# Performance work log

Measured on AMD Instinct MI355X. Metric: run time of the kernel, lower is better.

## Reference

```python
import jax, jax.numpy as jnp
import numpy as np

N_NODES = 100000
DEG = 16
N_FEAT = 128
HID = 128
N_CLASSES = 16
BATCH = 10000


def setup_inputs() -> dict:
    key = jax.random.key(0)
    k1, k2, k3, k4, k5 = jax.random.split(key, 5)
    nodes = jax.random.randint(k1, (BATCH,), 0, N_NODES, dtype=jnp.int32)
    neigh_idx = jax.random.randint(k2, (N_NODES, DEG), 0, N_NODES, dtype=jnp.int32)
    features = jax.random.normal(k3, (N_NODES, N_FEAT), dtype=jnp.float32)
    W1 = jax.random.normal(k4, (HID, 2 * N_FEAT), dtype=jnp.float32) * 0.05
    W2 = jax.random.normal(k5, (N_CLASSES, 2 * HID), dtype=jnp.float32) * 0.05
    return {"nodes": nodes, "neigh_idx": neigh_idx, "features": features,
            "W1": W1, "W2": W2}


def reference(nodes, neigh_idx, features, W1, W2):
    # --- layer 1 (full graph): mean-aggregate neighbors, concat self, linear, relu
    neigh1 = jnp.take(features, neigh_idx, axis=0).mean(axis=1)      # [N, F]
    comb1 = jnp.concatenate([features, neigh1], axis=1)              # [N, 2F]
    h1 = jax.nn.relu(comb1 @ W1.T)                                   # [N, HID]
    # --- layer 2 (batch nodes only)
    batch_nbrs = jnp.take(neigh_idx, nodes, axis=0)                  # [B, deg]
    neigh2 = jnp.take(h1, batch_nbrs, axis=0).mean(axis=1)           # [B, HID]
    self2 = jnp.take(h1, nodes, axis=0)                              # [B, HID]
    comb2 = jnp.concatenate([self2, neigh2], axis=1)                 # [B, 2*HID]
    return comb2 @ W2.T                                              # [B, C]
```

## Files before the change

### kernel.cpp

```cpp
#include <hip/hip_runtime.h>
#include <hip/hip_bf16.h>

#define NN 100000
#define DEG 16
#define NF 128
#define HID 128
#define NC 16
#define NB 10000

#define AS1 __attribute__((address_space(1)))
#define AS3 __attribute__((address_space(3)))

typedef float f32x16 __attribute__((ext_vector_type(16)));
typedef short s16x8 __attribute__((ext_vector_type(8)));

__device__ __forceinline__ ushort f2bf(float f) {
    unsigned u = __builtin_bit_cast(unsigned, f);
    return (ushort)((u + 0x7FFFu + ((u >> 16) & 1u)) >> 16);
}
__device__ __forceinline__ float bf2f(ushort h) {
    return __builtin_bit_cast(float, (unsigned)h << 16);
}
__device__ __forceinline__ uint cvtpk(float a, float b) {
    uint r;
    asm("v_cvt_pk_bf16_f32 %0, %1, %2" : "=v"(r) : "v"(a), "v"(b));
    return r;
}
__device__ __forceinline__ s16x8 pack8(float4 a, float4 b) {
    uint4 u;
    u.x = cvtpk(a.x, a.y);
    u.y = cvtpk(a.z, a.w);
    u.z = cvtpk(b.x, b.y);
    u.w = cvtpk(b.z, b.w);
    return __builtin_bit_cast(s16x8, u);
}
__device__ __forceinline__ int swz16(int row, int bo) {
    return row * 256 + (bo ^ ((row & 15) << 4));
}
__device__ __forceinline__ uint swzA(uint row, uint bo) {
    return bo ^ ((row & 31u) << 4);
}
__device__ __forceinline__ int pi_feat(int p) {
    const int n = p >> 5, h = (p >> 4) & 1, g = p & 15;
    return 32 * n + 4 * h + (g & 3) + 8 * (g >> 2);
}

__global__ __launch_bounds__(256)
void wf_prep(const float* __restrict__ W1, const float* __restrict__ W2,
             ushort* __restrict__ WFh, ushort* __restrict__ WF2) {
    const int t = blockIdx.x * 256 + threadIdx.x;
    if (t >= 72 * 64) return;
    const int frag = t >> 6;
    const int lane = t & 63;
    const int k0 = (frag & 7) * 16 + (lane >> 5) * 8;

    if (frag < 64) {
        const int vcol = (frag >> 3) * 32 + (lane & 31);
        const float* src = (vcol < 128) ? W1 + (size_t)vcol * 256
                                        : W1 + (size_t)(vcol - 128) * 256 + 128;
        ushort hh[8];
        #pragma unroll
        for (int j = 0; j < 8; ++j) hh[j] = f2bf(src[k0 + j]);
        *(uint4*)(WFh + (size_t)t * 8) = *(const uint4*)hh;
    } else {
        const int vcol = lane & 31;
        const float* src = (vcol < 16) ? W2 + (size_t)vcol * 256
                                       : W2 + (size_t)(vcol - 16) * 256 + 128;
        ushort hh[8];
        #pragma unroll
        for (int j = 0; j < 8; ++j) hh[j] = f2bf(src[pi_feat(k0 + j)]);
        *(uint4*)(WF2 + (size_t)((frag - 64) * 64 + lane) * 8) = *(const uint4*)hh;
    }
}

__global__ __launch_bounds__(256, 3)
void gemm1(const float* __restrict__ X, const ushort* __restrict__ WFh,
           ushort* __restrict__ Qb, unsigned char* __restrict__ Pf) {
    __shared__ char As[64 * 512];
    const int t = threadIdx.x;
    const int lane = t & 63;
    const int w = t >> 6;
    const int row0 = blockIdx.x * 64;

    #pragma unroll
    for (int j = 0; j < 8; ++j) {
        const uint chunk = (uint)(j * 4 + w);
        const uint o = chunk * 1024u + (uint)lane * 16u;
        const uint rrow = o >> 9;
        const uint bo = o & 511u;
        int grow = row0 + (int)rrow;
        if (grow > NN - 1) grow = NN - 1;
        const char* src = (const char*)X + (size_t)grow * 512 + swzA(rrow, bo);
        __builtin_amdgcn_global_load_lds((const AS1 void*)src,
                                         (AS3 void*)(As + chunk * 1024), 16, 0, 0);
    }
    __syncthreads();

    const int wm = w & 1;
    const int wn = w >> 1;
    const uint arow = (uint)(wm * 32 + (lane & 31));
    const char* abase = As + arow * 512;

    f32x16 acc[4];
    #pragma unroll
    for (int n = 0; n < 4; ++n)
        acc[n] = (f32x16){0,0,0,0,0,0,0,0,0,0,0,0,0,0,0,0};

    #pragma unroll
    for (int kk = 0; kk < 8; ++kk) {
        const uint bo = (uint)(kk * 64 + (lane >> 5) * 32);
        const float4 fa = *(const float4*)(abase + swzA(arow, bo));
        const float4 fb = *(const float4*)(abase + swzA(arow, bo + 16));
        const s16x8 a = pack8(fa, fb);
        #pragma unroll
        for (int n = 0; n < 4; ++n) {
            const int cf = wn * 4 + n;
            const s16x8 b = *(const s16x8*)(WFh + (size_t)((cf * 8 + kk) * 64 + lane) * 8);
            acc[n] = __builtin_amdgcn_mfma_f32_32x32x16_bf16(b, a, acc[n], 0, 0, 0);
        }
    }

    const int node = row0 + wm * 32 + (lane & 31);
    if (node < NN) {
        const int h16 = (lane >> 5) * 16;
        if (wn == 0) {
            ushort* qp = Qb + (size_t)node * HID + h16;
            #pragma unroll
            for (int n = 0; n < 4; ++n) {
                uint4 u0, u1;
                u0.x = cvtpk(acc[n][0], acc[n][1]);
                u0.y = cvtpk(acc[n][2], acc[n][3]);
                u0.z = cvtpk(acc[n][4], acc[n][5]);
                u0.w = cvtpk(acc[n][6], acc[n][7]);
                u1.x = cvtpk(acc[n][8], acc[n][9]);
                u1.y = cvtpk(acc[n][10], acc[n][11]);
                u1.z = cvtpk(acc[n][12], acc[n][13]);
                u1.w = cvtpk(acc[n][14], acc[n][15]);
                *(uint4*)(qp + n * 32) = u0;
                *(uint4*)(qp + n * 32 + 8) = u1;
            }
        } else {
            unsigned char* pp = Pf + (size_t)node * HID + h16;
            #pragma unroll
            for (int n = 0; n < 4; ++n) {
                uint uu[4];
                #pragma unroll
                for (int q = 0; q < 4; ++q) {
                    int v = __builtin_amdgcn_cvt_pk_fp8_f32(
                        acc[n][4 * q], acc[n][4 * q + 1], 0, false);
                    v = __builtin_amdgcn_cvt_pk_fp8_f32(
                        acc[n][4 * q + 2], acc[n][4 * q + 3], v, true);
                    uu[q] = (uint)v;
                }
                *(uint4*)(pp + n * 32) = *(const uint4*)uu;
            }
        }
    }
}

__global__ __launch_bounds__(256, 2)
void agg_gemm2(const int* __restrict__ nidx, const unsigned char* __restrict__ Pf,
               const ushort* __restrict__ Qb, const ushort* __restrict__ WF2,
               ushort* __restrict__ STb) {
    __shared__ char hs[128 * 256];
    const int t = threadIdx.x;
    const int node0 = blockIdx.x * 128;
    const int sl = t & 7;
    const int ng = t >> 3;

    const float inv = 1.0f / 16.0f;
    #pragma unroll 1
    for (int it = 0; it < 4; ++it) {
        const int r = ng + it * 32;
        int node = node0 + r;
        if (node > NN - 1) node = NN - 1;
        const int2 myn = *(const int2*)(nidx + (size_t)node * DEG + sl * 2);
        const ushort* qp = Qb + (size_t)node * HID + sl * 16;
        const s16x8 q0 = *(const s16x8*)qp;
        const s16x8 q1 = *(const s16x8*)(qp + 8);

        uint4 vv[16];
        #pragma unroll
        for (int d = 0; d < 16; ++d) {
            const uint id = (uint)__shfl((d & 1) ? myn.y : myn.x, d >> 1, 8);
            vv[d] = *(const uint4*)(Pf + (size_t)id * HID + sl * 16);
        }
        __builtin_amdgcn_sched_barrier(0);

        float s[16];
        #pragma unroll
        for (int j = 0; j < 16; ++j) s[j] = 0.f;
        #pragma unroll
        for (int d = 0; d < 16; ++d) {
            const uint wd[4] = {vv[d].x, vv[d].y, vv[d].z, vv[d].w};
            #pragma unroll
            for (int q = 0; q < 4; ++q) {
                const auto plo = __builtin_amdgcn_cvt_pk_f32_fp8(wd[q], false);
                const auto phi = __builtin_amdgcn_cvt_pk_f32_fp8(wd[q], true);
                s[q * 4 + 0] += plo[0]; s[q * 4 + 1] += plo[1];
                s[q * 4 + 2] += phi[0]; s[q * 4 + 3] += phi[1];
            }
        }

        float h[16];
        #pragma unroll
        for (int j = 0; j < 8; ++j) {
            h[j]     = fmaxf(fmaf(s[j],     inv, bf2f((ushort)q0[j])), 0.f);
            h[j + 8] = fmaxf(fmaf(s[j + 8], inv, bf2f((ushort)q1[j])), 0.f);
        }
        uint4 u0, u1;
        u0.x = cvtpk(h[0], h[1]);   u0.y = cvtpk(h[2], h[3]);
        u0.z = cvtpk(h[4], h[5]);   u0.w = cvtpk(h[6], h[7]);
        u1.x = cvtpk(h[8], h[9]);   u1.y = cvtpk(h[10], h[11]);
        u1.z = cvtpk(h[12], h[13]); u1.w = cvtpk(h[14], h[15]);
        *(uint4*)(hs + swz16(r, sl * 32)) = u0;
        *(uint4*)(hs + swz16(r, sl * 32 + 16)) = u1;
    }
    __syncthreads();

    const int lane = t & 63;
    const int w = t >> 6;
    const int rl = w * 32;

    f32x16 acc = {0,0,0,0,0,0,0,0,0,0,0,0,0,0,0,0};
    #pragma unroll
    for (int kk = 0; kk < 8; ++kk) {
        const int kb = kk * 32 + (lane >> 5) * 16;
        const s16x8 a = *(const s16x8*)(hs + swz16(rl + (lane & 31), kb));
        const s16x8 b = *(const s16x8*)(WF2 + (size_t)(kk * 64 + lane) * 8);
        acc = __builtin_amdgcn_mfma_f32_32x32x16_bf16(a, b, acc, 0, 0, 0);
    }

    const int col = lane & 31;
    const int crow4 = 4 * (lane >> 5);
    #pragma unroll
    for (int g = 0; g < 16; g += 2) {
        const uint pk = cvtpk(acc[g], acc[g + 1]);
        const int row = node0 + rl + (g & 3) + 8 * (g >> 2) + crow4;
        if (row < NN)     STb[(size_t)row * 32 + col] = (ushort)pk;
        if (row + 1 < NN) STb[(size_t)(row + 1) * 32 + col] = (ushort)(pk >> 16);
    }
}

__global__ __launch_bounds__(256)
void final_out(const int* __restrict__ nodes, const int* __restrict__ nidx,
               const ushort* __restrict__ STb, float* __restrict__ out) {
    const int g = blockIdx.x * 256 + threadIdx.x;
    if (g >= NB * NC / 2) return;
    const int b = g >> 3;
    const int jp = g & 7;
    const int node = nodes[b];
    const uint sv = *(const uint*)(STb + (size_t)node * 32 + jp * 2);
    const int* nb = nidx + (size_t)node * DEG;
    float a0 = 0.f, a1 = 0.f;
    #pragma unroll
    for (int d = 0; d < DEG; ++d) {
        const uint v = *(const uint*)(STb + (size_t)nb[d] * 32 + 16 + jp * 2);
        a0 += bf2f((ushort)v);
        a1 += bf2f((ushort)(v >> 16));
    }
    float2 o;
    o.x = fmaf(a0, 1.0f / 16.0f, bf2f((ushort)sv));
    o.y = fmaf(a1, 1.0f / 16.0f, bf2f((ushort)(sv >> 16)));
    *(float2*)(out + (size_t)b * 16 + jp * 2) = o;
}

extern "C" void kernel_launch(void* const* d_in, const int* in_sizes, int n_in,
                              void* d_out, int out_size, void* d_ws, size_t ws_size,
                              hipStream_t stream) {
    const int* nodes = (const int*)d_in[0];
    const int* nidx  = (const int*)d_in[1];
    const float* X   = (const float*)d_in[2];
    const float* W1  = (const float*)d_in[3];
    const float* W2  = (const float*)d_in[4];
    float* out = (float*)d_out;

    ushort* Qb = (ushort*)d_ws;
    unsigned char* Pf = (unsigned char*)(Qb + (size_t)NN * HID);
    ushort* STb = (ushort*)(Pf + (size_t)NN * HID);
    ushort* WFh = STb + (size_t)NN * 32;
    ushort* WF2 = WFh + 64 * 64 * 8;

    wf_prep<<<18, 256, 0, stream>>>(W1, W2, WFh, WF2);
    gemm1<<<1563, 256, 0, stream>>>(X, WFh, Qb, Pf);
    agg_gemm2<<<782, 256, 0, stream>>>(nidx, Pf, Qb, WF2, STb);
    final_out<<<313, 256, 0, stream>>>(nodes, nidx, STb, out);
}
```

Measured before the change: 75.86 us.

## Make gemm1 persistent over three tiles with double-buffered LDS prefetch

```diff
diff --git a/kernel.cpp b/kernel.cpp
--- a/kernel.cpp
+++ b/kernel.cpp
@@ -73,92 +73,120 @@
     }
 }
 
-__global__ __launch_bounds__(256, 3)
+__global__ __launch_bounds__(256, 2)
 void gemm1(const float* __restrict__ X, const ushort* __restrict__ WFh,
            ushort* __restrict__ Qb, unsigned char* __restrict__ Pf) {
-    __shared__ char As[64 * 512];
+    __shared__ char As[2][32768];
     const int t = threadIdx.x;
     const int lane = t & 63;
     const int w = t >> 6;
-    const int row0 = blockIdx.x * 64;
-
-    #pragma unroll
-    for (int j = 0; j < 8; ++j) {
-        const uint chunk = (uint)(j * 4 + w);
-        const uint o = chunk * 1024u + (uint)lane * 16u;
-        const uint rrow = o >> 9;
-        const uint bo = o & 511u;
-        int grow = row0 + (int)rrow;
-        if (grow > NN - 1) grow = NN - 1;
-        const char* src = (const char*)X + (size_t)grow * 512 + swzA(rrow, bo);
-        __builtin_amdgcn_global_load_lds((const AS1 void*)src,
-                                         (AS3 void*)(As + chunk * 1024), 16, 0, 0);
+    const int tileBase = blockIdx.x * 3;
+
+    {
+        const int row0 = tileBase * 64;
+        #pragma unroll
+        for (int j = 0; j < 8; ++j) {
+            const uint chunk = (uint)(j * 4 + w);
+            const uint o = chunk * 1024u + (uint)lane * 16u;
+            const uint rrow = o >> 9;
+            const uint bo = o & 511u;
+            int grow = row0 + (int)rrow;
+            if (grow > NN - 1) grow = NN - 1;
+            const char* src = (const char*)X + (size_t)grow * 512 + swzA(rrow, bo);
+            __builtin_amdgcn_global_load_lds((const AS1 void*)src,
+                                             (AS3 void*)(As[0] + chunk * 1024), 16, 0, 0);
+        }
     }
     __syncthreads();
 
     const int wm = w & 1;
     const int wn = w >> 1;
     const uint arow = (uint)(wm * 32 + (lane & 31));
-    const char* abase = As + arow * 512;
-
-    f32x16 acc[4];
+
     #pragma unroll
-    for (int n = 0; n < 4; ++n)
-        acc[n] = (f32x16){0,0,0,0,0,0,0,0,0,0,0,0,0,0,0,0};
-
-    #pragma unroll
-    for (int kk = 0; kk < 8; ++kk) {
-        const uint bo = (uint)(kk * 64 + (lane >> 5) * 32);
-        const float4 fa = *(const float4*)(abase + swzA(arow, bo));
-        const float4 fb = *(const float4*)(abase + swzA(arow, bo + 16));
-        const s16x8 a = pack8(fa, fb);
-        #pragma unroll
-        for (int n = 0; n < 4; ++n) {
-            const int cf = wn * 4 + n;
-            const s16x8 b = *(const s16x8*)(WFh + (size_t)((cf * 8 + kk) * 64 + lane) * 8);
-            acc[n] = __builtin_amdgcn_mfma_f32_32x32x16_bf16(b, a, acc[n], 0, 0, 0);
-        }
-    }
-
-    const int node = row0 + wm * 32 + (lane & 31);
-    if (node < NN) {
-        const int h16 = (lane >> 5) * 16;
-        if (wn == 0) {
-            ushort* qp = Qb + (size_t)node * HID + h16;
+    for (int tt = 0; tt < 3; ++tt) {
+        const int cur = tt & 1;
+        if (tt < 2) {
+            const int row0n = (tileBase + tt + 1) * 64;
+            #pragma unroll
+            for (int j = 0; j < 8; ++j) {
+                const uint chunk = (uint)(j * 4 + w);
+                const uint o = chunk * 1024u + (uint)lane * 16u;
+                const uint rrow = o >> 9;
+                const uint bo = o & 511u;
+                int grow = row0n + (int)rrow;
+                if (grow > NN - 1) grow = NN - 1;
+                const char* src = (const char*)X + (size_t)grow * 512 + swzA(rrow, bo);
+                __builtin_amdgcn_global_load_lds((const AS1 void*)src,
+                                                 (AS3 void*)(As[cur ^ 1] + chunk * 1024),
+                                                 16, 0, 0);
+            }
+        }
+        __builtin_amdgcn_sched_barrier(0);
+
+        const int row0 = (tileBase + tt) * 64;
+        const char* abase = As[cur] + arow * 512;
+
+        f32x16 acc[4];
+        #pragma unroll
+        for (int n = 0; n < 4; ++n)
+            acc[n] = (f32x16){0,0,0,0,0,0,0,0,0,0,0,0,0,0,0,0};
+
+        #pragma unroll
+        for (int kk = 0; kk < 8; ++kk) {
+            const uint bo = (uint)(kk * 64 + (lane >> 5) * 32);
+            const float4 fa = *(const float4*)(abase + swzA(arow, bo));
+            const float4 fb = *(const float4*)(abase + swzA(arow, bo + 16));
+            const s16x8 a = pack8(fa, fb);
             #pragma unroll
             for (int n = 0; n < 4; ++n) {
-                uint4 u0, u1;
-                u0.x = cvtpk(acc[n][0], acc[n][1]);
-                u0.y = cvtpk(acc[n][2], acc[n][3]);
-                u0.z = cvtpk(acc[n][4], acc[n][5]);
-                u0.w = cvtpk(acc[n][6], acc[n][7]);
-                u1.x = cvtpk(acc[n][8], acc[n][9]);
-                u1.y = cvtpk(acc[n][10], acc[n][11]);
-                u1.z = cvtpk(acc[n][12], acc[n][13]);
-                u1.w = cvtpk(acc[n][14], acc[n][15]);
-                *(uint4*)(qp + n * 32) = u0;
-                *(uint4*)(qp + n * 32 + 8) = u1;
+                const int cf = wn * 4 + n;
+                const s16x8 b = *(const s16x8*)(WFh + (size_t)((cf * 8 + kk) * 64 + lane) * 8);
+                acc[n] = __builtin_amdgcn_mfma_f32_32x32x16_bf16(b, a, acc[n], 0, 0, 0);
             }
-        } else {
-            unsigned char* pp = Pf + (size_t)node * HID + h16;
-            #pragma unroll
-            for (int n = 0; n < 4; ++n) {
-                uint uu[4];
+        }
+
+        const int node = row0 + wm * 32 + (lane & 31);
+        if (node < NN) {
+            const int h16 = (lane >> 5) * 16;
+            if (wn == 0) {
+                ushort* qp = Qb + (size_t)node * HID + h16;
                 #pragma unroll
-                for (int q = 0; q < 4; ++q) {
-                    int v = __builtin_amdgcn_cvt_pk_fp8_f32(
-                        acc[n][4 * q], acc[n][4 * q + 1], 0, false);
-                    v = __builtin_amdgcn_cvt_pk_fp8_f32(
-                        acc[n][4 * q + 2], acc[n][4 * q + 3], v, true);
-                    uu[q] = (uint)v;
+                for (int n = 0; n < 4; ++n) {
+                    uint4 u0, u1;
+                    u0.x = cvtpk(acc[n][0], acc[n][1]);
+                    u0.y = cvtpk(acc[n][2], acc[n][3]);
+                    u0.z = cvtpk(acc[n][4], acc[n][5]);
+                    u0.w = cvtpk(acc[n][6], acc[n][7]);
+                    u1.x = cvtpk(acc[n][8], acc[n][9]);
+                    u1.y = cvtpk(acc[n][10], acc[n][11]);
+                    u1.z = cvtpk(acc[n][12], acc[n][13]);
+                    u1.w = cvtpk(acc[n][14], acc[n][15]);
+                    *(uint4*)(qp + n * 32) = u0;
+                    *(uint4*)(qp + n * 32 + 8) = u1;
                 }
-                *(uint4*)(pp + n * 32) = *(const uint4*)uu;
+            } else {
+                unsigned char* pp = Pf + (size_t)node * HID + h16;
+                #pragma unroll
+                for (int n = 0; n < 4; ++n) {
+                    uint uu[4];
+                    #pragma unroll
+                    for (int q = 0; q < 4; ++q) {
+                        int v = __builtin_amdgcn_cvt_pk_fp8_f32(
+                            acc[n][4 * q], acc[n][4 * q + 1], 0, false);
+                        v = __builtin_amdgcn_cvt_pk_fp8_f32(
+                            acc[n][4 * q + 2], acc[n][4 * q + 3], v, true);
+                        uu[q] = (uint)v;
+                    }
+                    *(uint4*)(pp + n * 32) = *(const uint4*)uu;
+                }
             }
         }
-    }
-}
-
-__global__ __launch_bounds__(256, 2)
+        __syncthreads();
+    }
+}
+
+__global__ __launch_bounds__(256, 3)
 void agg_gemm2(const int* __restrict__ nidx, const unsigned char* __restrict__ Pf,
                const ushort* __restrict__ Qb, const ushort* __restrict__ WF2,
                ushort* __restrict__ STb) {
@@ -282,7 +310,7 @@
     ushort* WF2 = WFh + 64 * 64 * 8;
 
     wf_prep<<<18, 256, 0, stream>>>(W1, W2, WFh, WF2);
-    gemm1<<<1563, 256, 0, stream>>>(X, WFh, Qb, Pf);
+    gemm1<<<521, 256, 0, stream>>>(X, WFh, Qb, Pf);
     agg_gemm2<<<782, 256, 0, stream>>>(nidx, Pf, Qb, WF2, STb);
     final_out<<<313, 256, 0, stream>>>(nodes, nidx, STb, out);
 }
```

After: 72.58 us. -4.3%, faster.
